# Kernel tuning notes

Measured on AMD Instinct MI355X. Metric: run time of the kernel, lower is better.

The kernel has to match this reference:

```python
import jax, jax.numpy as jnp
import numpy as np

B, F0, K = 256, 40, 32          # batch, num fields, embedding dim
CIN_SIZE = [200, 200]            # layer widths (field_num[1:])


def setup_inputs() -> dict:
    key = jax.random.key(0)
    ks = jax.random.split(key, 1 + 4 * len(CIN_SIZE))
    field_num = [F0] + CIN_SIZE
    d = {"inputs": jax.random.normal(ks[0], (B, F0, K), dtype=jnp.float32)}
    for i in range(len(CIN_SIZE)):
        # W_query: (1, Fi, K); W_key/W_value: (1, F0, K); cin_W: (1, F0*Fi, F_{i+1})
        d[f"wq{i}"] = jax.random.normal(ks[1 + 4 * i], (1, field_num[i], K), dtype=jnp.float32) * 0.05
        d[f"wk{i}"] = jax.random.normal(ks[2 + 4 * i], (1, F0, K), dtype=jnp.float32) * 0.05
        d[f"wv{i}"] = jax.random.normal(ks[3 + 4 * i], (1, F0, K), dtype=jnp.float32) * 0.05
        lim = (6.0 / (F0 * field_num[i] + field_num[i + 1])) ** 0.5  # glorot uniform
        d[f"cw{i}"] = jax.random.uniform(ks[4 + 4 * i], (1, F0 * field_num[i], field_num[i + 1]),
                                         minval=-lim, maxval=lim, dtype=jnp.float32)
    return d


def _cin(inputs, params):
    # inputs: [B, F0, K]; params: list of (wq, wk, wv, cw) per CIN layer
    Bb, F0_, Kk = inputs.shape
    res = inputs
    outs = []
    for (wq, wk, wv, cw) in params:
        x0_wk = inputs * wk                 # [B, F0, K]
        x0_wv = inputs * wv                 # [B, F0, K]
        xi_wq = res * wq                    # [B, Fi, K]
        # per-embedding-slot outer product scores: phi[b,k,f0,fi]
        phi = jnp.einsum('bfk,bgk->bkfg', x0_wk, xi_wq)
        # exp + normalize over F0 axis == softmax over axis=2
        alpha = jax.nn.softmax(phi, axis=2)                      # [B, K, F0, Fi]
        x = alpha * jnp.transpose(x0_wv, (0, 2, 1))[:, :, :, None]  # [B, K, F0, Fi]
        x = x.reshape(Bb, Kk, -1)           # flatten (f0, fi) row-major -> f0*Fi + fi
        # conv1d with kernel width 1 == channel matmul: [B, K, F0*Fi] @ [F0*Fi, F_{i+1}]
        out = jnp.einsum('bkc,cj->bjk', x, cw[0])                # [B, F_{i+1}, K]
        outs.append(out)
        res = out
    cat = jnp.concatenate(outs, axis=1)     # [B, sum(cin_size), K]
    return cat.sum(axis=-1)                 # [B, sum(cin_size)]


def reference(inputs, wq0, wk0, wv0, cw0, wq1, wk1, wv1, cw1):
    return _cin(inputs, [(wq0, wk0, wv0, cw0), (wq1, wk1, wv1, cw1)])
```

## Files before the change

### kernel.cpp

```cpp
#include <hip/hip_runtime.h>
#include <hip/hip_bf16.h>


#define NF0   40
#define KD    32
#define NJ    200
#define NTILE 14
#define NTHR  512

typedef short bf16x8 __attribute__((ext_vector_type(8)));
typedef float f32x4  __attribute__((ext_vector_type(4)));
typedef unsigned short u16;
typedef unsigned int   u32;

static __device__ __forceinline__ u16 f2bf(float f) {
    __hip_bfloat16 h = __float2bfloat16(f);
    return *reinterpret_cast<u16*>(&h);
}
static __device__ __forceinline__ float bf2f(u16 u) {
    u32 x = ((u32)u) << 16;
    float f;
    __builtin_memcpy(&f, &x, 4);
    return f;
}

template<int FI, int FIP>
__global__ __launch_bounds__(256)
void pack_b(const float* __restrict__ cw, u16* __restrict__ bp) {
    constexpr int G = FIP * NF0 / 32;
    int t = blockIdx.x * 256 + threadIdx.x;
    if (t >= NTILE * G * 64) return;
    const int lane = t & 63;
    const int g    = (t >> 6) % G;
    const int nt   = t / (64 * G);
    const int j    = nt * 16 + (lane & 15);
    const int cb   = g * 32 + (lane >> 4) * 8;
    u16 v[8];
    #pragma unroll
    for (int i = 0; i < 8; ++i) {
        int cp = cb + i;
        int fi = cp / NF0;
        int f0 = cp - fi * NF0;
        float x = (j < NJ && fi < FI) ? cw[(size_t)(f0 * FI + fi) * NJ + j] : 0.0f;
        v[i] = f2bf(x);
    }
    *reinterpret_cast<bf16x8*>(bp + (size_t)t * 8) = *reinterpret_cast<const bf16x8*>(v);
}

template<int FI, int NBATCH, int NSPLIT, int FIR, int MT, bool RESBF16>
__global__ __launch_bounds__(NTHR)
void cin_layer(const float* __restrict__ x0,
               const float* __restrict__ resf,
               const u16*  __restrict__ resb,
               const float* __restrict__ wq,
               const float* __restrict__ wk,
               const float* __restrict__ wv,
               const u16* __restrict__ bp,
               u16* __restrict__ res_out,
               float* __restrict__ out)
{
    constexpr int M     = NBATCH * 32;
    constexpr int NCH   = FIR / 4;
    constexpr int G     = NSPLIT * FIR * NF0 / 32;
    constexpr int XROWB = 384;

    __shared__ float s_stage[NBATCH * 2560 + NBATCH * FIR * 32];
    __shared__ u16   s_XT[M * 192];

    float* s_xk = s_stage;
    float* s_xv = s_stage + NBATCH * 1280;
    float* s_q  = s_stage + NBATCH * 2560;

    const int tid   = threadIdx.x;
    const int b0    = (blockIdx.x / NSPLIT) * NBATCH;
    const int split = blockIdx.x % NSPLIT;
    const int wid   = tid >> 6, lane = tid & 63;
    const int wrow  = lane & 15, wq4 = lane >> 4;
    const int mg    = wid & 3,  ng  = wid >> 2;

    if constexpr (NSPLIT > 1) {
        if (split == 0) {
            for (int idx = tid; idx < NBATCH * NJ; idx += NTHR) {
                int bb = idx / NJ, j = idx - bb * NJ;
                const u16* rp = resb + (size_t)(b0 + bb) * (NJ * KD) + j * KD;
                float s = 0.f;
                #pragma unroll
                for (int q8 = 0; q8 < 4; ++q8) {
                    bf16x8 v = *reinterpret_cast<const bf16x8*>(rp + q8 * 8);
                    #pragma unroll
                    for (int i = 0; i < 8; ++i) s += bf2f((u16)v[i]);
                }
                out[(size_t)(b0 + bb) * 400 + j] = s;
            }
        }
    }

    for (int idx = tid; idx < NBATCH * 1280; idx += NTHR) {
        int bb = idx / 1280, r = idx - bb * 1280;
        float v = x0[(size_t)(b0 + bb) * 1280 + r];
        s_xk[idx] = v * wk[r];
        s_xv[idx] = v * wv[r];
    }
    for (int idx = tid; idx < NBATCH * FIR * 32; idx += NTHR) {
        int bb = idx / (FIR * 32);
        int rr = idx - bb * (FIR * 32);
        int fi = split * FIR + (rr >> 5);
        int k  = rr & 31;
        float qv = 0.f;
        if (fi < FI) {
            float rv;
            if constexpr (RESBF16)
                rv = bf2f(resb[(size_t)(b0 + bb) * (FI * KD) + fi * KD + k]);
            else
                rv = resf[(size_t)(b0 + bb) * (FI * KD) + fi * KD + k];
            qv = rv * wq[fi * KD + k];
        }
        s_q[idx] = qv;
    }
    __syncthreads();

    f32x4 acc[MT][7];
    #pragma unroll
    for (int mt = 0; mt < MT; ++mt)
        #pragma unroll
        for (int t = 0; t < 7; ++t)
            acc[mt][t] = (f32x4){0.f, 0.f, 0.f, 0.f};

    const int gbase = split * (FIR * NF0 / 32);

    for (int ch = 0; ch < NCH; ++ch) {
        if (tid < NBATCH * 128) {
            const int bb  = tid >> 7;
            const int fil = (tid >> 5) & 3;
            const int k   = tid & 31;
            const int fig = split * FIR + ch * 4 + fil;
            const int row = bb * 32 + k;
            char* rbase = (char*)s_XT + row * XROWB;
            const int swx = (row & 7) << 4;
            if (fig < FI) {
                const float qv = s_q[(bb * FIR + ch * 4 + fil) * 32 + k];
                const float* xkp = s_xk + bb * 1280 + k;
                const float* xvp = s_xv + bb * 1280 + k;
                float e[NF0];
                float d = 0.f;
                #pragma unroll
                for (int f0 = 0; f0 < NF0; ++f0) {
                    e[f0] = __expf(xkp[f0 * 32] * qv);
                    d += e[f0];
                }
                const float r = 1.0f / d;
                #pragma unroll
                for (int p = 0; p < 20; ++p) {
                    u32 w = (u32)f2bf(e[2*p]   * r * xvp[(2*p)   * 32])
                          | ((u32)f2bf(e[2*p+1] * r * xvp[(2*p+1) * 32]) << 16);
                    *reinterpret_cast<u32*>(rbase + ((fil * 80 + p * 4) ^ swx)) = w;
                }
            } else {
                #pragma unroll
                for (int p = 0; p < 20; ++p)
                    *reinterpret_cast<u32*>(rbase + ((fil * 80 + p * 4) ^ swx)) = 0u;
            }
        }
        __syncthreads();

        #pragma unroll
        for (int ks = 0; ks < 5; ++ks) {
            bf16x8 a[MT];
            #pragma unroll
            for (int mt = 0; mt < MT; ++mt) {
                const int row = (mg * MT + mt) * 16 + wrow;
                a[mt] = *reinterpret_cast<const bf16x8*>(
                    (char*)s_XT + row * XROWB + ((ks * 64 + wq4 * 16) ^ ((row & 7) << 4)));
            }
            const int gg = gbase + ch * 5 + ks;
            #pragma unroll
            for (int t = 0; t < 7; ++t) {
                const int nt = ng * 7 + t;
                bf16x8 bb = *reinterpret_cast<const bf16x8*>(
                    bp + ((size_t)(nt * G + gg) * 64 + lane) * 8);
                #pragma unroll
                for (int mt = 0; mt < MT; ++mt)
                    acc[mt][t] = __builtin_amdgcn_mfma_f32_16x16x32_bf16(a[mt], bb, acc[mt][t], 0, 0, 0);
            }
        }
        __syncthreads();
    }

    if constexpr (NSPLIT == 1) {
        const int mrow = mg * 16 + wq4 * 4;
        const int bb = mrow >> 5;
        const int kk = mrow & 31;
        #pragma unroll
        for (int t = 0; t < 7; ++t) {
            const int j = (ng * 7 + t) * 16 + wrow;
            if (j < NJ) {
                u16 pk[4];
                #pragma unroll
                for (int r = 0; r < 4; ++r) pk[r] = f2bf(acc[0][t][r]);
                *reinterpret_cast<unsigned long long*>(
                    res_out + (size_t)(b0 + bb) * (NJ * KD) + j * KD + kk)
                    = *reinterpret_cast<const unsigned long long*>(pk);
            }
        }
    } else {
        #pragma unroll
        for (int t = 0; t < 7; ++t) {
            float s = 0.f;
            #pragma unroll
            for (int mt = 0; mt < MT; ++mt)
                #pragma unroll
                for (int r = 0; r < 4; ++r) s += acc[mt][t][r];
            s += __shfl_xor(s, 16);
            s += __shfl_xor(s, 32);
            const int j = (ng * 7 + t) * 16 + wrow;
            if (wq4 == 0 && j < NJ)
                atomicAdd(&out[(size_t)(b0 + mg) * 400 + 200 + j], s);
        }
    }
}

extern "C" void kernel_launch(void* const* d_in, const int* in_sizes, int n_in,
                              void* d_out, int out_size, void* d_ws, size_t ws_size,
                              hipStream_t stream) {
    const float* x0  = (const float*)d_in[0];
    const float* wq0 = (const float*)d_in[1];
    const float* wk0 = (const float*)d_in[2];
    const float* wv0 = (const float*)d_in[3];
    const float* cw0 = (const float*)d_in[4];
    const float* wq1 = (const float*)d_in[5];
    const float* wk1 = (const float*)d_in[6];
    const float* wv1 = (const float*)d_in[7];
    const float* cw1 = (const float*)d_in[8];
    float* out = (float*)d_out;

    char* ws = (char*)d_ws;
    u16* res = (u16*)ws;
    u16* bp0 = (u16*)(ws + 3276800);
    u16* bp1 = (u16*)(ws + 3276800 + 716800);

    hipMemsetAsync(d_out, 0, (size_t)out_size * 4, stream);

    pack_b<40, 40>  <<<175, 256, 0, stream>>>(cw0, bp0);
    pack_b<200, 208><<<910, 256, 0, stream>>>(cw1, bp1);

    cin_layer<40, 2, 1, 40, 1, false><<<128, NTHR, 0, stream>>>(
        x0, x0, nullptr, wq0, wk0, wv0, bp0, res, nullptr);

    cin_layer<200, 4, 4, 52, 2, true><<<256, NTHR, 0, stream>>>(
        x0, nullptr, res, wq1, wk1, wv1, bp1, nullptr, out);
}
```

Measured before the change: 223.3 us.

## Re-partition CIN layers for more blocks and coalesce weight packing via LDS tile

Layer 0 now runs one batch per block split across two N halves (512 blocks), and layer 1 uses two batches per block (512 blocks) instead of four. All 512 threads now share the softmax staging by splitting the F0 reduction in halves joined with a shuffle. The weight pack kernel reads coalesced float4 rows through a shared tile rather than strided scalar loads. MFMA sections get raised wave priority. The goal is better occupancy, more active CUs, and better use of threads in the exp phase, at the cost of reloading B fragments across more blocks.

```diff
diff --git a/kernel.cpp b/kernel.cpp
--- a/kernel.cpp
+++ b/kernel.cpp
@@ -12,6 +12,7 @@
 typedef float f32x4  __attribute__((ext_vector_type(4)));
 typedef unsigned short u16;
 typedef unsigned int   u32;
+typedef unsigned long long u64;
 
 static __device__ __forceinline__ u16 f2bf(float f) {
     __hip_bfloat16 h = __float2bfloat16(f);
@@ -24,197 +25,250 @@
     return f;
 }
 
-template<int FI, int FIP>
+template<int FI>
 __global__ __launch_bounds__(256)
-void pack_b(const float* __restrict__ cw, u16* __restrict__ bp) {
-    constexpr int G = FIP * NF0 / 32;
-    int t = blockIdx.x * 256 + threadIdx.x;
-    if (t >= NTILE * G * 64) return;
-    const int lane = t & 63;
-    const int g    = (t >> 6) % G;
-    const int nt   = t / (64 * G);
-    const int j    = nt * 16 + (lane & 15);
-    const int cb   = g * 32 + (lane >> 4) * 8;
-    u16 v[8];
+void pack_b(const float* __restrict__ cw, u16* __restrict__ bp, int G) {
+    __shared__ float tile[64][17];
+    const int band = blockIdx.x, nt = blockIdx.y;
+    const int t = threadIdx.x;
+    {
+        const int cl = t >> 2, qj = t & 3;
+        const int cp = band * 64 + cl;
+        const int fi = cp / NF0, f0 = cp - fi * NF0;
+        const int j0 = nt * 16 + qj * 4;
+        float4 v = make_float4(0.f, 0.f, 0.f, 0.f);
+        if (fi < FI) {
+            const float* src = cw + (size_t)(f0 * FI + fi) * NJ + j0;
+            if (j0 + 3 < NJ) v = *reinterpret_cast<const float4*>(src);
+            else {
+                if (j0 + 0 < NJ) v.x = src[0];
+                if (j0 + 1 < NJ) v.y = src[1];
+                if (j0 + 2 < NJ) v.z = src[2];
+                if (j0 + 3 < NJ) v.w = src[3];
+            }
+        }
+        tile[cl][qj * 4 + 0] = v.x;
+        tile[cl][qj * 4 + 1] = v.y;
+        tile[cl][qj * 4 + 2] = v.z;
+        tile[cl][qj * 4 + 3] = v.w;
+    }
+    __syncthreads();
+    if (t < 128) {
+        const int g2 = t >> 6, lane = t & 63;
+        const int jl = lane & 15, c8 = g2 * 32 + (lane >> 4) * 8;
+        u16 v[8];
+        #pragma unroll
+        for (int i = 0; i < 8; ++i) v[i] = f2bf(tile[c8 + i][jl]);
+        *reinterpret_cast<bf16x8*>(bp + ((size_t)(nt * G + band * 2 + g2) * 64 + lane) * 8)
+            = *reinterpret_cast<const bf16x8*>(v);
+    }
+}
+
+__global__ __launch_bounds__(NTHR, 4)
+void cin_layer0(const float* __restrict__ x0,
+                const float* __restrict__ wq, const float* __restrict__ wk,
+                const float* __restrict__ wv,
+                const u16* __restrict__ bp, u16* __restrict__ res) {
+    constexpr int G0 = 50;
+    __shared__ float s_xk[1280], s_xv[1280], s_q[1280];
+    __shared__ u16 s_XT[32 * 384];
+
+    const int tid = threadIdx.x;
+    const int b = blockIdx.x >> 1, js = blockIdx.x & 1;
+    const int wid = tid >> 6, lane = tid & 63;
+    const int wrow = lane & 15, wq4 = lane >> 4;
+    const int mg = wid & 1, ng = wid >> 1;
+
+    for (int i = tid; i < 1280; i += NTHR) {
+        float v = x0[(size_t)b * 1280 + i];
+        s_xk[i] = v * wk[i];
+        s_xv[i] = v * wv[i];
+        s_q[i]  = v * wq[i];
+    }
+    __syncthreads();
+
+    f32x4 acc[2];
     #pragma unroll
-    for (int i = 0; i < 8; ++i) {
-        int cp = cb + i;
-        int fi = cp / NF0;
-        int f0 = cp - fi * NF0;
-        float x = (j < NJ && fi < FI) ? cw[(size_t)(f0 * FI + fi) * NJ + j] : 0.0f;
-        v[i] = f2bf(x);
-    }
-    *reinterpret_cast<bf16x8*>(bp + (size_t)t * 8) = *reinterpret_cast<const bf16x8*>(v);
-}
-
-template<int FI, int NBATCH, int NSPLIT, int FIR, int MT, bool RESBF16>
-__global__ __launch_bounds__(NTHR)
-void cin_layer(const float* __restrict__ x0,
-               const float* __restrict__ resf,
-               const u16*  __restrict__ resb,
-               const float* __restrict__ wq,
-               const float* __restrict__ wk,
-               const float* __restrict__ wv,
-               const u16* __restrict__ bp,
-               u16* __restrict__ res_out,
-               float* __restrict__ out)
-{
-    constexpr int M     = NBATCH * 32;
-    constexpr int NCH   = FIR / 4;
-    constexpr int G     = NSPLIT * FIR * NF0 / 32;
-    constexpr int XROWB = 384;
-
-    __shared__ float s_stage[NBATCH * 2560 + NBATCH * FIR * 32];
-    __shared__ u16   s_XT[M * 192];
-
-    float* s_xk = s_stage;
-    float* s_xv = s_stage + NBATCH * 1280;
-    float* s_q  = s_stage + NBATCH * 2560;
-
-    const int tid   = threadIdx.x;
-    const int b0    = (blockIdx.x / NSPLIT) * NBATCH;
-    const int split = blockIdx.x % NSPLIT;
-    const int wid   = tid >> 6, lane = tid & 63;
-    const int wrow  = lane & 15, wq4 = lane >> 4;
-    const int mg    = wid & 3,  ng  = wid >> 2;
-
-    if constexpr (NSPLIT > 1) {
-        if (split == 0) {
-            for (int idx = tid; idx < NBATCH * NJ; idx += NTHR) {
-                int bb = idx / NJ, j = idx - bb * NJ;
-                const u16* rp = resb + (size_t)(b0 + bb) * (NJ * KD) + j * KD;
-                float s = 0.f;
+    for (int t = 0; t < 2; ++t) acc[t] = (f32x4){0.f, 0.f, 0.f, 0.f};
+
+    const int sfil = tid >> 6, sh = (tid >> 5) & 1, sk = tid & 31;
+    char* srb = (char*)s_XT + sk * 768;
+    const int sswx = (sk & 7) << 4;
+    const int arow = mg * 16 + wrow;
+    char* apb = (char*)s_XT + arow * 768;
+    const int aswx = (arow & 7) << 4;
+
+    for (int ch = 0; ch < 5; ++ch) {
+        {
+            const float qv = s_q[(ch * 8 + sfil) * 32 + sk];
+            const float* xkp = s_xk + sh * 640 + sk;
+            const float* xvp = s_xv + sh * 640 + sk;
+            float e[20];
+            float d = 0.f;
+            #pragma unroll
+            for (int i = 0; i < 20; ++i) {
+                e[i] = __expf(xkp[i * 32] * qv);
+                d += e[i];
+            }
+            d += __shfl_xor(d, 32);
+            const float r = 1.0f / d;
+            #pragma unroll
+            for (int p = 0; p < 10; ++p) {
+                u32 w = (u32)f2bf(e[2 * p] * r * xvp[(2 * p) * 32])
+                      | ((u32)f2bf(e[2 * p + 1] * r * xvp[(2 * p + 1) * 32]) << 16);
+                *reinterpret_cast<u32*>(srb + ((sfil * 80 + sh * 40 + p * 4) ^ sswx)) = w;
+            }
+        }
+        __syncthreads();
+        __builtin_amdgcn_s_setprio(1);
+        #pragma unroll
+        for (int ks = 0; ks < 10; ++ks) {
+            bf16x8 a = *reinterpret_cast<const bf16x8*>(apb + ((ks * 64 + wq4 * 16) ^ aswx));
+            const int g = ch * 10 + ks;
+            #pragma unroll
+            for (int t = 0; t < 2; ++t) {
+                const int ntl = ng * 2 + t;
+                if (ntl < 7) {
+                    const int nt = js * 7 + ntl;
+                    bf16x8 bfr = *reinterpret_cast<const bf16x8*>(
+                        bp + ((size_t)(nt * G0 + g) * 64 + lane) * 8);
+                    acc[t] = __builtin_amdgcn_mfma_f32_16x16x32_bf16(a, bfr, acc[t], 0, 0, 0);
+                }
+            }
+        }
+        __builtin_amdgcn_s_setprio(0);
+        __syncthreads();
+    }
+
+    const int kbase = mg * 16 + wq4 * 4;
+    #pragma unroll
+    for (int t = 0; t < 2; ++t) {
+        const int ntl = ng * 2 + t;
+        if (ntl < 7) {
+            const int j = (js * 7 + ntl) * 16 + wrow;
+            if (j < NJ) {
+                u16 pk[4];
                 #pragma unroll
-                for (int q8 = 0; q8 < 4; ++q8) {
-                    bf16x8 v = *reinterpret_cast<const bf16x8*>(rp + q8 * 8);
-                    #pragma unroll
-                    for (int i = 0; i < 8; ++i) s += bf2f((u16)v[i]);
-                }
-                out[(size_t)(b0 + bb) * 400 + j] = s;
-            }
-        }
-    }
-
-    for (int idx = tid; idx < NBATCH * 1280; idx += NTHR) {
-        int bb = idx / 1280, r = idx - bb * 1280;
+                for (int r = 0; r < 4; ++r) pk[r] = f2bf(acc[t][r]);
+                *reinterpret_cast<u64*>(res + (size_t)b * (NJ * KD) + j * KD + kbase)
+                    = *reinterpret_cast<const u64*>(pk);
+            }
+        }
+    }
+}
+
+__global__ __launch_bounds__(NTHR, 4)
+void cin_layer1(const float* __restrict__ x0, const u16* __restrict__ resb,
+                const float* __restrict__ wq, const float* __restrict__ wk,
+                const float* __restrict__ wv,
+                const u16* __restrict__ bp, float* __restrict__ out) {
+    constexpr int G1 = 260, FIR = 52;
+    __shared__ float s_xk[2560], s_xv[2560], s_q[2 * FIR * 32];
+    __shared__ u16 s_XT[64 * 192];
+
+    const int tid = threadIdx.x;
+    const int bg = blockIdx.x >> 2, split = blockIdx.x & 3;
+    const int b0 = bg * 2;
+    const int wid = tid >> 6, lane = tid & 63;
+    const int wrow = lane & 15, wq4 = lane >> 4;
+    const int mg = wid & 3, ng = wid >> 2;
+
+    if (split == 0) {
+        for (int idx = tid; idx < 2 * NJ; idx += NTHR) {
+            const int bb = idx / NJ, j = idx - bb * NJ;
+            const u16* rp = resb + (size_t)(b0 + bb) * (NJ * KD) + j * KD;
+            float s = 0.f;
+            #pragma unroll
+            for (int q8 = 0; q8 < 4; ++q8) {
+                bf16x8 v = *reinterpret_cast<const bf16x8*>(rp + q8 * 8);
+                #pragma unroll
+                for (int i = 0; i < 8; ++i) s += bf2f((u16)v[i]);
+            }
+            out[(size_t)(b0 + bb) * 400 + j] = s;
+        }
+    }
+
+    for (int idx = tid; idx < 2560; idx += NTHR) {
+        const int bb = idx / 1280, r = idx - bb * 1280;
         float v = x0[(size_t)(b0 + bb) * 1280 + r];
         s_xk[idx] = v * wk[r];
         s_xv[idx] = v * wv[r];
     }
-    for (int idx = tid; idx < NBATCH * FIR * 32; idx += NTHR) {
-        int bb = idx / (FIR * 32);
-        int rr = idx - bb * (FIR * 32);
-        int fi = split * FIR + (rr >> 5);
-        int k  = rr & 31;
+    for (int idx = tid; idx < 2 * FIR * 32; idx += NTHR) {
+        const int bb = idx / (FIR * 32), rr = idx - bb * (FIR * 32);
+        const int fi = split * FIR + (rr >> 5), k = rr & 31;
         float qv = 0.f;
-        if (fi < FI) {
-            float rv;
-            if constexpr (RESBF16)
-                rv = bf2f(resb[(size_t)(b0 + bb) * (FI * KD) + fi * KD + k]);
-            else
-                rv = resf[(size_t)(b0 + bb) * (FI * KD) + fi * KD + k];
-            qv = rv * wq[fi * KD + k];
-        }
+        if (fi < 200)
+            qv = bf2f(resb[(size_t)(b0 + bb) * (NJ * KD) + fi * KD + k]) * wq[fi * KD + k];
         s_q[idx] = qv;
     }
     __syncthreads();
 
-    f32x4 acc[MT][7];
+    f32x4 acc[7];
     #pragma unroll
-    for (int mt = 0; mt < MT; ++mt)
-        #pragma unroll
-        for (int t = 0; t < 7; ++t)
-            acc[mt][t] = (f32x4){0.f, 0.f, 0.f, 0.f};
-
-    const int gbase = split * (FIR * NF0 / 32);
-
-    for (int ch = 0; ch < NCH; ++ch) {
-        if (tid < NBATCH * 128) {
-            const int bb  = tid >> 7;
-            const int fil = (tid >> 5) & 3;
-            const int k   = tid & 31;
-            const int fig = split * FIR + ch * 4 + fil;
-            const int row = bb * 32 + k;
-            char* rbase = (char*)s_XT + row * XROWB;
-            const int swx = (row & 7) << 4;
-            if (fig < FI) {
-                const float qv = s_q[(bb * FIR + ch * 4 + fil) * 32 + k];
-                const float* xkp = s_xk + bb * 1280 + k;
-                const float* xvp = s_xv + bb * 1280 + k;
-                float e[NF0];
-                float d = 0.f;
-                #pragma unroll
-                for (int f0 = 0; f0 < NF0; ++f0) {
-                    e[f0] = __expf(xkp[f0 * 32] * qv);
-                    d += e[f0];
-                }
-                const float r = 1.0f / d;
-                #pragma unroll
-                for (int p = 0; p < 20; ++p) {
-                    u32 w = (u32)f2bf(e[2*p]   * r * xvp[(2*p)   * 32])
-                          | ((u32)f2bf(e[2*p+1] * r * xvp[(2*p+1) * 32]) << 16);
-                    *reinterpret_cast<u32*>(rbase + ((fil * 80 + p * 4) ^ swx)) = w;
-                }
-            } else {
-                #pragma unroll
-                for (int p = 0; p < 20; ++p)
-                    *reinterpret_cast<u32*>(rbase + ((fil * 80 + p * 4) ^ swx)) = 0u;
-            }
+    for (int t = 0; t < 7; ++t) acc[t] = (f32x4){0.f, 0.f, 0.f, 0.f};
+
+    const int sbb = tid >> 8, sfil = (tid >> 6) & 3, sh = (tid >> 5) & 1, sk = tid & 31;
+    const int srow = sbb * 32 + sk;
+    char* srb = (char*)s_XT + srow * 384;
+    const int sswx = (srow & 7) << 4;
+    const int arow = mg * 16 + wrow;
+    char* apb = (char*)s_XT + arow * 384;
+    const int aswx = (arow & 7) << 4;
+
+    for (int ch = 0; ch < 13; ++ch) {
+        const int fig = split * FIR + ch * 4 + sfil;
+        if (fig < 200) {
+            const float qv = s_q[sbb * (FIR * 32) + (ch * 4 + sfil) * 32 + sk];
+            const float* xkp = s_xk + sbb * 1280 + sh * 640 + sk;
+            const float* xvp = s_xv + sbb * 1280 + sh * 640 + sk;
+            float e[20];
+            float d = 0.f;
+            #pragma unroll
+            for (int i = 0; i < 20; ++i) {
+                e[i] = __expf(xkp[i * 32] * qv);
+                d += e[i];
+            }
+            d += __shfl_xor(d, 32);
+            const float r = 1.0f / d;
+            #pragma unroll
+            for (int p = 0; p < 10; ++p) {
+                u32 w = (u32)f2bf(e[2 * p] * r * xvp[(2 * p) * 32])
+                      | ((u32)f2bf(e[2 * p + 1] * r * xvp[(2 * p + 1) * 32]) << 16);
+                *reinterpret_cast<u32*>(srb + ((sfil * 80 + sh * 40 + p * 4) ^ sswx)) = w;
+            }
+        } else {
+            #pragma unroll
+            for (int p = 0; p < 10; ++p)
+                *reinterpret_cast<u32*>(srb + ((sfil * 80 + sh * 40 + p * 4) ^ sswx)) = 0u;
         }
         __syncthreads();
-
+        __builtin_amdgcn_s_setprio(1);
         #pragma unroll
         for (int ks = 0; ks < 5; ++ks) {
-            bf16x8 a[MT];
-            #pragma unroll
-            for (int mt = 0; mt < MT; ++mt) {
-                const int row = (mg * MT + mt) * 16 + wrow;
-                a[mt] = *reinterpret_cast<const bf16x8*>(
-                    (char*)s_XT + row * XROWB + ((ks * 64 + wq4 * 16) ^ ((row & 7) << 4)));
-            }
-            const int gg = gbase + ch * 5 + ks;
+            bf16x8 a = *reinterpret_cast<const bf16x8*>(apb + ((ks * 64 + wq4 * 16) ^ aswx));
+            const int g = split * 65 + ch * 5 + ks;
             #pragma unroll
             for (int t = 0; t < 7; ++t) {
-                const int nt = ng * 7 + t;
-                bf16x8 bb = *reinterpret_cast<const bf16x8*>(
-                    bp + ((size_t)(nt * G + gg) * 64 + lane) * 8);
-                #pragma unroll
-                for (int mt = 0; mt < MT; ++mt)
-                    acc[mt][t] = __builtin_amdgcn_mfma_f32_16x16x32_bf16(a[mt], bb, acc[mt][t], 0, 0, 0);
-            }
-        }
+                const int nt2 = ng * 7 + t;
+                bf16x8 bfr = *reinterpret_cast<const bf16x8*>(
+                    bp + ((size_t)(nt2 * G1 + g) * 64 + lane) * 8);
+                acc[t] = __builtin_amdgcn_mfma_f32_16x16x32_bf16(a, bfr, acc[t], 0, 0, 0);
+            }
+        }
+        __builtin_amdgcn_s_setprio(0);
         __syncthreads();
     }
 
-    if constexpr (NSPLIT == 1) {
-        const int mrow = mg * 16 + wq4 * 4;
-        const int bb = mrow >> 5;
-        const int kk = mrow & 31;
-        #pragma unroll
-        for (int t = 0; t < 7; ++t) {
-            const int j = (ng * 7 + t) * 16 + wrow;
-            if (j < NJ) {
-                u16 pk[4];
-                #pragma unroll
-                for (int r = 0; r < 4; ++r) pk[r] = f2bf(acc[0][t][r]);
-                *reinterpret_cast<unsigned long long*>(
-                    res_out + (size_t)(b0 + bb) * (NJ * KD) + j * KD + kk)
-                    = *reinterpret_cast<const unsigned long long*>(pk);
-            }
-        }
-    } else {
-        #pragma unroll
-        for (int t = 0; t < 7; ++t) {
-            float s = 0.f;
-            #pragma unroll
-            for (int mt = 0; mt < MT; ++mt)
-                #pragma unroll
-                for (int r = 0; r < 4; ++r) s += acc[mt][t][r];
-            s += __shfl_xor(s, 16);
-            s += __shfl_xor(s, 32);
-            const int j = (ng * 7 + t) * 16 + wrow;
-            if (wq4 == 0 && j < NJ)
-                atomicAdd(&out[(size_t)(b0 + mg) * 400 + 200 + j], s);
+    #pragma unroll
+    for (int t = 0; t < 7; ++t) {
+        float s = acc[t][0] + acc[t][1] + acc[t][2] + acc[t][3];
+        s += __shfl_xor(s, 16);
+        s += __shfl_xor(s, 32);
+        const int j = (ng * 7 + t) * 16 + wrow;
+        if (wq4 == 0 && j < NJ) {
+            const int bb = mg >> 1;
+            atomicAdd(&out[(size_t)(b0 + bb) * 400 + 200 + j], s);
         }
     }
 }
@@ -240,12 +294,9 @@
 
     hipMemsetAsync(d_out, 0, (size_t)out_size * 4, stream);
 
-    pack_b<40, 40>  <<<175, 256, 0, stream>>>(cw0, bp0);
-    pack_b<200, 208><<<910, 256, 0, stream>>>(cw1, bp1);
-
-    cin_layer<40, 2, 1, 40, 1, false><<<128, NTHR, 0, stream>>>(
-        x0, x0, nullptr, wq0, wk0, wv0, bp0, res, nullptr);
-
-    cin_layer<200, 4, 4, 52, 2, true><<<256, NTHR, 0, stream>>>(
-        x0, nullptr, res, wq1, wk1, wv1, bp1, nullptr, out);
-}
+    pack_b<40> <<<dim3(25, NTILE), 256, 0, stream>>>(cw0, bp0, 50);
+    pack_b<200><<<dim3(130, NTILE), 256, 0, stream>>>(cw1, bp1, 260);
+
+    cin_layer0<<<512, NTHR, 0, stream>>>(x0, wq0, wk0, wv0, bp0, res);
+    cin_layer1<<<512, NTHR, 0, stream>>>(x0, res, wq1, wk1, wv1, bp1, out);
+}
```

Result: faster. 199.8 us (-10.5%).
